# Performance work log

Hardware: AMD Instinct MI355X
Metric: run time of the kernel (lower is better)

Reference implementation:

```python
import jax, jax.numpy as jnp
import numpy as np

NFFT = 1024
N_FREQ = NFFT // 2  # 512


def _ifft_kernels():
    # Intended kernels: exp(1j * 2*pi * t * f / nfft), columns 1..nfft/2,
    # scaled by 2 except the Nyquist column (last) which keeps weight 1.
    t = np.arange(NFFT, dtype=np.float64)[:, None]          # [1024, 1]
    f = np.arange(1, N_FREQ + 1, dtype=np.float64)[None, :]  # [1, 512]
    ang = 2.0 * np.pi * t * f / float(NFFT)
    real_k = 2.0 * np.cos(ang)
    imag_k = 2.0 * np.sin(ang)
    real_k[:, -1] /= 2.0
    imag_k[:, -1] /= 2.0
    return real_k.astype(np.float32), imag_k.astype(np.float32)


def setup_inputs() -> dict:
    key = jax.random.key(0)
    k1, k2 = jax.random.split(key)
    B, T = 8, 4096
    magn = jax.random.normal(k1, (B, 1, N_FREQ, T), dtype=jnp.float32)
    phase = jax.random.normal(k2, (B, 1, N_FREQ, T), dtype=jnp.float32)
    rk, ik = _ifft_kernels()
    return {
        "magn": magn,
        "phase": phase,
        "real_kernels": jnp.asarray(rk),   # [1024, 512]
        "imag_kernels": jnp.asarray(ik),   # [1024, 512]
    }


def reference(magn, phase, real_kernels, imag_kernels):
    # Conv2d(1, nfft, (n_freq, 1)) over [B,1,F,T] == dense matmul over freq axis.
    # out[b, c, t] = sum_f W[c, f] * x[b, f, t]
    m = magn[:, 0]   # [B, F, T]
    p = phase[:, 0]  # [B, F, T]
    out = jnp.einsum('cf,bft->bct', real_kernels, m) \
        - jnp.einsum('cf,bft->bct', imag_kernels, p)
    out = out[:, :, None, :] / NFFT  # [B, nfft, 1, T]
    return out
```

## Files before the change

kernel.cpp:

```cpp
#include <hip/hip_runtime.h>
#include <hip/hip_bf16.h>

#define NFREQ 512
#define KDIM  1024
#define CDIM  1024
#define TDIM  4096
#define BATCH 8
#define NT    16

typedef __bf16 bf16;
typedef __attribute__((ext_vector_type(8))) __bf16 bf16x8;
typedef __attribute__((ext_vector_type(4))) float f32x4;

__device__ __forceinline__ void gload_lds16(const bf16* g, void* l) {
    __builtin_amdgcn_global_load_lds(
        (const __attribute__((address_space(1))) void*)g,
        (__attribute__((address_space(3))) void*)l, 16, 0, 0);
}

__global__ __launch_bounds__(256) void prep_kc(const float* __restrict__ rk,
                                               const float* __restrict__ ik,
                                               bf16* __restrict__ Kc) {
    int idx = blockIdx.x * 256 + threadIdx.x;
    int c = idx >> 10;
    int k = idx & 1023;
    float v = (k < NFREQ) ? rk[c * NFREQ + k] : -ik[c * NFREQ + (k - NFREQ)];
    Kc[idx] = (bf16)(v * (1.0f / 1024.0f));
}

__global__ __launch_bounds__(256) void transpose_kernel(const float* __restrict__ magn,
                                                        const float* __restrict__ phase,
                                                        bf16* __restrict__ Xt) {
    __shared__ bf16 tile[64][68];
    const int tid = threadIdx.x;
    const int tt  = blockIdx.x & 63;
    const int ft  = blockIdx.x >> 6;
    const int b   = blockIdx.y;
    const int src = blockIdx.z;
    const float* in = src ? phase : magn;
    const int f0 = ft * 64, t0 = tt * 64;
    const size_t base = (size_t)b * NFREQ * TDIM;

    const int r0 = tid >> 4;
    const int c4 = (tid & 15) * 4;
#pragma unroll
    for (int i = 0; i < 4; i++) {
        int r = r0 + i * 16;
        const float4 v = *(const float4*)&in[base + (size_t)(f0 + r) * TDIM + t0 + c4];
        tile[r][c4 + 0] = (bf16)v.x;
        tile[r][c4 + 1] = (bf16)v.y;
        tile[r][c4 + 2] = (bf16)v.z;
        tile[r][c4 + 3] = (bf16)v.w;
    }
    __syncthreads();
    const int kbase = src * NFREQ + f0;
#pragma unroll
    for (int i = 0; i < 2; i++) {
        int ch = tid + 256 * i;
        int tr = ch >> 3;
        int c8 = (ch & 7) * 8;
        bf16x8 o;
#pragma unroll
        for (int j = 0; j < 8; j++) o[j] = tile[c8 + j][tr];
        *(bf16x8*)&Xt[((size_t)b * TDIM + t0 + tr) * KDIM + kbase + c8] = o;
    }
}

__global__ __launch_bounds__(512, 2) void gemm8(const bf16* __restrict__ Kc,
                                                const bf16* __restrict__ Xt,
                                                float* __restrict__ out) {
    extern __shared__ __align__(16) char smem[];

    const int tid = threadIdx.x;
    const int w = tid >> 6;
    const int l = tid & 63;

    const int bid = blockIdx.x;
    const int swz = ((bid & 7) << 3) | (bid >> 3);
    const int bm = swz >> 4;
    const int bn = swz & 15;
    const int b  = blockIdx.y;

    const bf16* Abase = Kc + (size_t)(bm * 256) * KDIM;
    const bf16* Bbase = Xt + ((size_t)b * TDIM + bn * 256) * KDIM;

    const int srow   = ((w >> 2) * 128) + ((w & 3) * 8);
    const int ssub   = l >> 3;
    const int scol   = ((l & 7) ^ ssub) * 8;

    const int wr = w >> 2;
    const int wc = w & 3;
    const int fr = l & 15;
    const int l16 = l >> 4;
    const int fx = fr & 7;

    f32x4 acc[8][4] = {};

#define STAGE_A(curb, q, kt) \
    gload_lds16(Abase + (size_t)(srow + (q)*32 + ssub) * KDIM + (kt)*64 + scol, \
                smem + (curb)*65536 + (srow + (q)*32) * 128)
#define STAGE_B(curb, q, kt) \
    gload_lds16(Bbase + (size_t)(srow + (q)*32 + ssub) * KDIM + (kt)*64 + scol, \
                smem + (curb)*65536 + 32768 + (srow + (q)*32) * 128)

#pragma unroll
    for (int q = 0; q < 4; q++) STAGE_A(0, q, 0);
#pragma unroll
    for (int q = 0; q < 4; q++) STAGE_B(0, q, 0);
    STAGE_A(1, 0, 1); STAGE_A(1, 1, 1); STAGE_A(1, 2, 1);
    asm volatile("s_waitcnt vmcnt(3)" ::: "memory");
    __builtin_amdgcn_s_barrier();
    __builtin_amdgcn_sched_barrier(0);

    for (int v = 0; v < NT; ++v) {
        const int cur = v & 1;
        const char* At = smem + cur * 65536;
        const char* Bt = At + 32768;
        bf16x8 bfr[4][2];

#pragma unroll
        for (int p = 0; p < 4; p++) {
            bf16x8 afr[2][2];
#pragma unroll
            for (int mi = 0; mi < 2; mi++)
#pragma unroll
                for (int kk = 0; kk < 2; kk++) {
                    const int r = wr * 128 + (p * 2 + mi) * 16 + fr;
                    const int off = r * 128 + (((kk * 4 + l16) ^ fx) * 16);
                    afr[mi][kk] = *(const bf16x8*)(At + off);
                }
            if (p == 0) {
#pragma unroll
                for (int n = 0; n < 4; n++)
#pragma unroll
                    for (int kk = 0; kk < 2; kk++) {
                        const int r = wc * 64 + n * 16 + fr;
                        const int off = r * 128 + (((kk * 4 + l16) ^ fx) * 16);
                        bfr[n][kk] = *(const bf16x8*)(Bt + off);
                    }
            }

            if (p == 0) {
                if (v + 1 < NT) {
                    const int nc = cur ^ 1;
                    STAGE_A(nc, 3, v + 1);
                    STAGE_B(nc, 0, v + 1); STAGE_B(nc, 1, v + 1);
                    STAGE_B(nc, 2, v + 1); STAGE_B(nc, 3, v + 1);
                }
            } else {
                if (v + 2 < NT) STAGE_A(cur, p - 1, v + 2);
            }

            __builtin_amdgcn_s_barrier();
            __builtin_amdgcn_s_setprio(1);
#pragma unroll
            for (int mi = 0; mi < 2; mi++)
#pragma unroll
                for (int n = 0; n < 4; n++)
#pragma unroll
                    for (int kk = 0; kk < 2; kk++)
                        acc[p * 2 + mi][n] = __builtin_amdgcn_mfma_f32_16x16x32_bf16(
                            afr[mi][kk], bfr[n][kk], acc[p * 2 + mi][n], 0, 0, 0);
            __builtin_amdgcn_s_setprio(0);
            if (p == 3) {
                if (v < NT - 2) { asm volatile("s_waitcnt vmcnt(3)" ::: "memory"); }
                else           { asm volatile("s_waitcnt vmcnt(0)" ::: "memory"); }
            }
            __builtin_amdgcn_s_barrier();
            __builtin_amdgcn_sched_barrier(0);
        }
    }
#undef STAGE_A
#undef STAGE_B

    const int cr = l16 * 4;
    const int cc = fr;
    float* obase = out + ((size_t)b * CDIM + bm * 256 + wr * 128) * TDIM + bn * 256 + wc * 64;
#pragma unroll
    for (int m = 0; m < 8; m++)
#pragma unroll
        for (int n = 0; n < 4; n++)
#pragma unroll
            for (int j = 0; j < 4; j++)
                obase[(size_t)(m * 16 + cr + j) * TDIM + n * 16 + cc] = acc[m][n][j];
}

__global__ __launch_bounds__(256) void naive_kernel(const float* __restrict__ m,
                                                    const float* __restrict__ p,
                                                    const float* __restrict__ rk,
                                                    const float* __restrict__ ik,
                                                    float* __restrict__ out) {
    size_t idx = (size_t)blockIdx.x * 256 + threadIdx.x;
    int t = idx & 4095;
    size_t r = idx >> 12;
    int c = (int)(r & 1023);
    int b = (int)(r >> 10);
    float acc = 0.f;
    for (int f = 0; f < NFREQ; f++) {
        acc += rk[c * NFREQ + f] * m[((size_t)b * NFREQ + f) * TDIM + t]
             - ik[c * NFREQ + f] * p[((size_t)b * NFREQ + f) * TDIM + t];
    }
    out[idx] = acc * (1.0f / 1024.0f);
}

extern "C" void kernel_launch(void* const* d_in, const int* in_sizes, int n_in,
                              void* d_out, int out_size, void* d_ws, size_t ws_size,
                              hipStream_t stream) {
    const float* magn  = (const float*)d_in[0];
    const float* phase = (const float*)d_in[1];
    const float* rk    = (const float*)d_in[2];
    const float* ik    = (const float*)d_in[3];
    float* out = (float*)d_out;

    const size_t kc_bytes = (size_t)CDIM * KDIM * sizeof(bf16);
    const size_t xt_bytes = (size_t)BATCH * TDIM * KDIM * sizeof(bf16);
    if (ws_size < kc_bytes + xt_bytes) {
        naive_kernel<<<(CDIM * TDIM * BATCH) / 256, 256, 0, stream>>>(magn, phase, rk, ik, out);
        return;
    }

    bf16* Kc = (bf16*)d_ws;
    bf16* Xt = (bf16*)((char*)d_ws + kc_bytes);

    (void)hipFuncSetAttribute((const void*)gemm8,
                              hipFuncAttributeMaxDynamicSharedMemorySize, 131072);

    prep_kc<<<(CDIM * KDIM) / 256, 256, 0, stream>>>(rk, ik, Kc);
    transpose_kernel<<<dim3(512, BATCH, 2), 256, 0, stream>>>(magn, phase, Xt);
    gemm8<<<dim3(64, BATCH), 512, 131072, stream>>>(Kc, Xt, out);
}
```

Baseline: 125.8 us.

## Make GEMM blocks compute two M tiles sequentially and remap grid

The GEMM grid shrinks from 512 to 256 blocks, and each block loops over two consecutive 256-row output tiles with the same batch and N tile. Block index decoding now puts batch in the low bits, so concurrently running blocks spread across batches. The aim is to match the grid to the CU count, roughly one block per CU, and avoid a partial second wave. The cost is that each block does twice the work serially, the B tile is reloaded for each M tile, and the pipeline prologue and epilogue are repeated within a block.

```diff
diff --git a/kernel.cpp b/kernel.cpp
--- a/kernel.cpp
+++ b/kernel.cpp
@@ -75,13 +75,12 @@
     const int w = tid >> 6;
     const int l = tid & 63;
 
-    const int bid = blockIdx.x;
-    const int swz = ((bid & 7) << 3) | (bid >> 3);
-    const int bm = swz >> 4;
-    const int bn = swz & 15;
-    const int b  = blockIdx.y;
-
-    const bf16* Abase = Kc + (size_t)(bm * 256) * KDIM;
+    const int g   = blockIdx.x;
+    const int b   = g & 7;
+    const int s   = g >> 3;
+    const int bn  = s & 15;
+    const int bmp = s >> 4;
+
     const bf16* Bbase = Xt + ((size_t)b * TDIM + bn * 256) * KDIM;
 
     const int srow   = ((w >> 2) * 128) + ((w & 3) * 8);
@@ -94,95 +93,109 @@
     const int l16 = l >> 4;
     const int fx = fr & 7;
 
-    f32x4 acc[8][4] = {};
+    f32x4 acc[8][4];
 
 #define STAGE_A(curb, q, kt) \
-    gload_lds16(Abase + (size_t)(srow + (q)*32 + ssub) * KDIM + (kt)*64 + scol, \
+    gload_lds16(Ab + (size_t)(srow + (q)*32 + ssub) * KDIM + (kt)*64 + scol, \
                 smem + (curb)*65536 + (srow + (q)*32) * 128)
 #define STAGE_B(curb, q, kt) \
     gload_lds16(Bbase + (size_t)(srow + (q)*32 + ssub) * KDIM + (kt)*64 + scol, \
                 smem + (curb)*65536 + 32768 + (srow + (q)*32) * 128)
 
-#pragma unroll
-    for (int q = 0; q < 4; q++) STAGE_A(0, q, 0);
-#pragma unroll
-    for (int q = 0; q < 4; q++) STAGE_B(0, q, 0);
-    STAGE_A(1, 0, 1); STAGE_A(1, 1, 1); STAGE_A(1, 2, 1);
-    asm volatile("s_waitcnt vmcnt(3)" ::: "memory");
-    __builtin_amdgcn_s_barrier();
-    __builtin_amdgcn_sched_barrier(0);
-
-    for (int v = 0; v < NT; ++v) {
-        const int cur = v & 1;
-        const char* At = smem + cur * 65536;
-        const char* Bt = At + 32768;
-        bf16x8 bfr[4][2];
-
-#pragma unroll
-        for (int p = 0; p < 4; p++) {
-            bf16x8 afr[2][2];
-#pragma unroll
-            for (int mi = 0; mi < 2; mi++)
-#pragma unroll
-                for (int kk = 0; kk < 2; kk++) {
-                    const int r = wr * 128 + (p * 2 + mi) * 16 + fr;
-                    const int off = r * 128 + (((kk * 4 + l16) ^ fx) * 16);
-                    afr[mi][kk] = *(const bf16x8*)(At + off);
+    for (int ti = 0; ti < 2; ++ti) {
+        const int bm = bmp * 2 + ti;
+        const bf16* Ab = Kc + (size_t)(bm * 256) * KDIM;
+
+#pragma unroll
+        for (int m = 0; m < 8; m++)
+#pragma unroll
+            for (int n = 0; n < 4; n++)
+                acc[m][n] = (f32x4){0.f, 0.f, 0.f, 0.f};
+
+#pragma unroll
+        for (int q = 0; q < 4; q++) STAGE_A(0, q, 0);
+#pragma unroll
+        for (int q = 0; q < 4; q++) STAGE_B(0, q, 0);
+        STAGE_A(1, 0, 1); STAGE_A(1, 1, 1); STAGE_A(1, 2, 1);
+        asm volatile("s_waitcnt vmcnt(3)" ::: "memory");
+        __builtin_amdgcn_s_barrier();
+        __builtin_amdgcn_sched_barrier(0);
+
+        for (int v = 0; v < NT; ++v) {
+            const int cur = v & 1;
+            const char* At = smem + cur * 65536;
+            const char* Bt = At + 32768;
+            bf16x8 bfr[4][2];
+
+#pragma unroll
+            for (int p = 0; p < 4; p++) {
+                bf16x8 afr[2][2];
+#pragma unroll
+                for (int mi = 0; mi < 2; mi++)
+#pragma unroll
+                    for (int kk = 0; kk < 2; kk++) {
+                        const int r = wr * 128 + (p * 2 + mi) * 16 + fr;
+                        const int off = r * 128 + (((kk * 4 + l16) ^ fx) * 16);
+                        afr[mi][kk] = *(const bf16x8*)(At + off);
+                    }
+                if (p == 0) {
+#pragma unroll
+                    for (int n = 0; n < 4; n++)
+#pragma unroll
+                        for (int kk = 0; kk < 2; kk++) {
+                            const int r = wc * 64 + n * 16 + fr;
+                            const int off = r * 128 + (((kk * 4 + l16) ^ fx) * 16);
+                            bfr[n][kk] = *(const bf16x8*)(Bt + off);
+                        }
                 }
-            if (p == 0) {
+
+                if (p == 0) {
+                    if (v + 1 < NT) {
+                        const int nc = cur ^ 1;
+                        STAGE_A(nc, 3, v + 1);
+                        STAGE_B(nc, 0, v + 1); STAGE_B(nc, 1, v + 1);
+                        STAGE_B(nc, 2, v + 1); STAGE_B(nc, 3, v + 1);
+                    }
+                } else {
+                    if (v + 2 < NT) STAGE_A(cur, p - 1, v + 2);
+                }
+
+                __builtin_amdgcn_s_barrier();
+                __builtin_amdgcn_s_setprio(1);
+#pragma unroll
+                for (int mi = 0; mi < 2; mi++)
+#pragma unroll
+                    for (int n = 0; n < 4; n++)
+#pragma unroll
+                        for (int kk = 0; kk < 2; kk++)
+                            acc[p * 2 + mi][n] = __builtin_amdgcn_mfma_f32_16x16x32_bf16(
+                                afr[mi][kk], bfr[n][kk], acc[p * 2 + mi][n], 0, 0, 0);
+                __builtin_amdgcn_s_setprio(0);
+                if (p == 3) {
+                    if (v < NT - 2) { asm volatile("s_waitcnt vmcnt(3)" ::: "memory"); }
+                    else            { asm volatile("s_waitcnt vmcnt(0)" ::: "memory"); }
+                }
+                __builtin_amdgcn_s_barrier();
+                __builtin_amdgcn_sched_barrier(0);
+            }
+        }
+
+        {
+            const int cr = l16 * 4;
+            const int cc = fr;
+            float* obase = out + ((size_t)b * CDIM + bm * 256 + wr * 128) * TDIM
+                               + bn * 256 + wc * 64;
+#pragma unroll
+            for (int m = 0; m < 8; m++)
 #pragma unroll
                 for (int n = 0; n < 4; n++)
 #pragma unroll
-                    for (int kk = 0; kk < 2; kk++) {
-                        const int r = wc * 64 + n * 16 + fr;
-                        const int off = r * 128 + (((kk * 4 + l16) ^ fx) * 16);
-                        bfr[n][kk] = *(const bf16x8*)(Bt + off);
-                    }
-            }
-
-            if (p == 0) {
-                if (v + 1 < NT) {
-                    const int nc = cur ^ 1;
-                    STAGE_A(nc, 3, v + 1);
-                    STAGE_B(nc, 0, v + 1); STAGE_B(nc, 1, v + 1);
-                    STAGE_B(nc, 2, v + 1); STAGE_B(nc, 3, v + 1);
-                }
-            } else {
-                if (v + 2 < NT) STAGE_A(cur, p - 1, v + 2);
-            }
-
-            __builtin_amdgcn_s_barrier();
-            __builtin_amdgcn_s_setprio(1);
-#pragma unroll
-            for (int mi = 0; mi < 2; mi++)
-#pragma unroll
-                for (int n = 0; n < 4; n++)
-#pragma unroll
-                    for (int kk = 0; kk < 2; kk++)
-                        acc[p * 2 + mi][n] = __builtin_amdgcn_mfma_f32_16x16x32_bf16(
-                            afr[mi][kk], bfr[n][kk], acc[p * 2 + mi][n], 0, 0, 0);
-            __builtin_amdgcn_s_setprio(0);
-            if (p == 3) {
-                if (v < NT - 2) { asm volatile("s_waitcnt vmcnt(3)" ::: "memory"); }
-                else           { asm volatile("s_waitcnt vmcnt(0)" ::: "memory"); }
-            }
-            __builtin_amdgcn_s_barrier();
-            __builtin_amdgcn_sched_barrier(0);
+                    for (int j = 0; j < 4; j++)
+                        obase[(size_t)(m * 16 + cr + j) * TDIM + n * 16 + cc] = acc[m][n][j];
         }
     }
 #undef STAGE_A
 #undef STAGE_B
-
-    const int cr = l16 * 4;
-    const int cc = fr;
-    float* obase = out + ((size_t)b * CDIM + bm * 256 + wr * 128) * TDIM + bn * 256 + wc * 64;
-#pragma unroll
-    for (int m = 0; m < 8; m++)
-#pragma unroll
-        for (int n = 0; n < 4; n++)
-#pragma unroll
-            for (int j = 0; j < 4; j++)
-                obase[(size_t)(m * 16 + cr + j) * TDIM + n * 16 + cc] = acc[m][n][j];
 }
 
 __global__ __launch_bounds__(256) void naive_kernel(const float* __restrict__ m,
@@ -227,5 +240,5 @@
 
     prep_kc<<<(CDIM * KDIM) / 256, 256, 0, stream>>>(rk, ik, Kc);
     transpose_kernel<<<dim3(512, BATCH, 2), 256, 0, stream>>>(magn, phase, Xt);
-    gemm8<<<dim3(64, BATCH), 512, 131072, stream>>>(Kc, Xt, out);
-}
+    gemm8<<<dim3(256), 512, 131072, stream>>>(Kc, Xt, out);
+}
```

After: 283.5 us. +125.4%, slower.
